# Performance work log

Hardware: AMD Instinct MI355X
Metric: run time of the kernel (lower is better)

Reference implementation:

```python
import jax, jax.numpy as jnp
import numpy as np

EPS = 1e-5  # BatchNorm eps (eval mode)
K_MAIN = 10
K_CORR = 8
LRELU = 0.2


def _knn_idx(x, k):
    # x: [B, c, n] -> [B, n, k] indices of k nearest neighbors (negative sq. distance top-k)
    inner = -2.0 * jnp.einsum('bcn,bcm->bnm', x, x)
    xx = jnp.sum(x * x, axis=1)                      # [B, n]
    pd = -xx[:, :, None] - inner - xx[:, None, :]    # [B, n, n]
    return jax.lax.top_k(pd, k)[1]


def _gather_neighbors(x, idx):
    # x: [B, c, n], idx: [B, n, k] -> [B, n, k, c]
    xt = jnp.transpose(x, (0, 2, 1))
    B = x.shape[0]
    return xt[jnp.arange(B)[:, None, None], idx]


def _graph_feature(x, k):
    # torch get_graph_feature: cat(neighbor - center, center) -> [B, 2c, n, k]
    idx = _knn_idx(x, k)
    neigh = _gather_neighbors(x, idx)                 # [B, n, k, c]
    xt = jnp.transpose(x, (0, 2, 1))                  # [B, n, c]
    center = jnp.broadcast_to(xt[:, :, None, :], neigh.shape)
    feat = jnp.concatenate([neigh - center, center], axis=-1)
    return jnp.transpose(feat, (0, 3, 1, 2))


def _branch(feat, w, g, b, m, v):
    # 1x1 Conv2d (no bias) + BatchNorm2d (eval) + LeakyReLU(0.2)
    y = jnp.einsum('oc,bcnk->bonk', w, feat)
    s = (g / jnp.sqrt(v + EPS))[None, :, None, None]
    y = (y - m[None, :, None, None]) * s + b[None, :, None, None]
    return jnp.where(y > 0, y, LRELU * y)


def _erase(x, masks, soft, w_e, b_e, g_e, be_e, m_e, v_e):
    # erase_feature: masked-softmax attention pooling + 1x1 conv_erase (conv+BN)
    soft = soft - (1.0 - masks) * 1e8
    sm = jax.nn.softmax(soft, axis=1)                 # [B, n]
    inp = x * masks[:, None, :]
    res = jnp.einsum('bcn,bn->bc', x, sm)             # [B, c]
    y = jnp.einsum('oc,bc->bo', w_e, res) + b_e
    y = (y - m_e) * (g_e / jnp.sqrt(v_e + EPS)) + be_e
    return inp + y[:, :, None]


def _corre_binar(x0_, x2, w_reduce):
    # x0_: [B, c] (detached query), x2: [B, c, n]
    B, c, n = x2.shape
    q = jnp.einsum('oc,bc->bo', w_reduce, x0_)        # conv_reduce (1x1, no bias)
    scale = 1.0 / jnp.sqrt(jnp.asarray(c, x2.dtype))
    f = jnp.einsum('bc,bcn->bn', q, x2) * scale       # [B, n]
    idx8 = _knn_idx(x2, K_CORR)                       # [B, n, 8]
    neigh = _gather_neighbors(x2, idx8)               # [B, n, 8, c]
    fk = jnp.einsum('bc,bnkc->bnk', q, neigh) * scale
    fk = f + jnp.sum(fk, axis=-1)                     # [B, n]
    index = jnp.argmax(fk, axis=1)                    # [B]
    ib = jnp.arange(B)
    masks = jnp.zeros((B, n), x2.dtype).at[ib, index].set(1.0)
    index_k = idx8[ib, index]                         # [B, 8] neighbors of argmax point
    masks = masks.at[ib[:, None], index_k].set(1.0)
    return 1.0 - masks, f


def _forward(x, w_reduce, w_erase, b_erase, g_erase, be_erase, m_erase, v_erase,
             w0, g0, b0, m0, v0, w1, g1, b1, m1, v1):
    b, t, c, n = x.shape
    B = b * t
    x1seq = jnp.concatenate([x[:, 1:], x[:, -1:]], axis=1).reshape(B, c, n)
    ones = jnp.ones((B, n), x.dtype)
    x0 = _erase(x.reshape(B, c, n), ones, ones,
                w_erase, b_erase, g_erase, be_erase, m_erase, v_erase)
    y0 = jnp.max(_branch(_graph_feature(x0, K_MAIN), w0, g0, b0, m0, v0), axis=-1)  # [B, O, n]
    x0_vec = jnp.max(y0, axis=-1)                                                    # [B, O]
    p0 = jnp.concatenate([jnp.max(y0, axis=-1), jnp.mean(y0, axis=-1)], axis=1)
    masks, soft = _corre_binar(jax.lax.stop_gradient(x0_vec), x1seq, w_reduce)
    x1e = _erase(x1seq, masks, soft,
                 w_erase, b_erase, g_erase, be_erase, m_erase, v_erase)
    y1 = jnp.max(_branch(_graph_feature(x1e, K_MAIN), w1, g1, b1, m1, v1), axis=-1)
    p1 = jnp.concatenate([jnp.max(y1, axis=-1), jnp.mean(y1, axis=-1)], axis=1)
    return p0 + p1                                                                   # [B, 2*O]


def setup_inputs() -> dict:
    key = jax.random.key(0)
    ks = jax.random.split(key, 20)
    b, t, c, n, out = 8, 12, 64, 512, 64
    sc = np.sqrt(2.0 / c).astype(np.float32)
    scb = np.sqrt(2.0 / out).astype(np.float32)
    f32 = jnp.float32
    inp = {
        'x': jax.random.normal(ks[0], (b, t, c, n), f32),
        'w_reduce': jax.random.normal(ks[1], (c, c), f32) * sc,
        'w_erase': jax.random.normal(ks[2], (c, c), f32) * sc,
        'b_erase': jax.random.normal(ks[3], (c,), f32) * 0.01,
        'g_erase': jax.random.uniform(ks[4], (c,), f32, 0.5, 1.5),
        'be_erase': jax.random.normal(ks[5], (c,), f32) * 0.1,
        'm_erase': jax.random.normal(ks[6], (c,), f32) * 0.1,
        'v_erase': jax.random.uniform(ks[7], (c,), f32, 0.5, 1.5),
        'w0': jax.random.normal(ks[8], (out, 2 * c), f32) * scb,
        'g0': jax.random.uniform(ks[9], (out,), f32, 0.5, 1.5),
        'b0': jax.random.normal(ks[10], (out,), f32) * 0.1,
        'm0': jax.random.normal(ks[11], (out,), f32) * 0.1,
        'v0': jax.random.uniform(ks[12], (out,), f32, 0.5, 1.5),
        'w1': jax.random.normal(ks[13], (out, 2 * c), f32) * scb,
        'g1': jax.random.uniform(ks[14], (out,), f32, 0.5, 1.5),
        'b1': jax.random.normal(ks[15], (out,), f32) * 0.1,
        'm1': jax.random.normal(ks[16], (out,), f32) * 0.1,
        'v1': jax.random.uniform(ks[17], (out,), f32, 0.5, 1.5),
    }
    return inp


def reference(x, w_reduce, w_erase, b_erase, g_erase, be_erase, m_erase, v_erase,
              w0, g0, b0, m0, v0, w1, g1, b1, m1, v1):
    return _forward(x, w_reduce, w_erase, b_erase, g_erase, be_erase, m_erase, v_erase,
                    w0, g0, b0, m0, v0, w1, g1, b1, m1, v1)
```

## Files before the change

kernel.cpp:

```cpp
#include <hip/hip_runtime.h>
#include <math.h>

#define EPS 1e-5f

typedef _Float16 half8 __attribute__((ext_vector_type(8)));
typedef float f32x4 __attribute__((ext_vector_type(4)));


__device__ __forceinline__ int src_row(int bq) {
    int b = bq / 12, t = bq - b * 12;
    int t2 = (t + 1 < 12) ? (t + 1) : 11;
    return b * 12 + t2;
}

__global__ __launch_bounds__(256) void prep_kernel(
    const float* __restrict__ X,
    _Float16* __restrict__ H, _Float16* __restrict__ L, float* __restrict__ xn,
    const float* __restrict__ w0, const float* __restrict__ w1,
    _Float16* __restrict__ wh0, _Float16* __restrict__ wl0,
    _Float16* __restrict__ wh1, _Float16* __restrict__ wl1,
    const float* __restrict__ w_e, const float* __restrict__ b_e,
    const float* __restrict__ g_e, const float* __restrict__ be_e,
    const float* __restrict__ m_e, const float* __restrict__ v_e,
    float* __restrict__ bias0)
{
    __shared__ float lds[64 * 65];
    __shared__ float xnp[4 * 64];
    __shared__ float part[256];
    __shared__ float res[64];
    __shared__ float sy[64];
    int raw = blockIdx.x;
    int tid = threadIdx.x;
    if (raw >= 768) {
        int bq = raw - 768;
        int c = tid >> 2, p = tid & 3;
        const float* xb = X + (size_t)bq * 32768 + c * 512 + p * 128;
        float acc = 0.f;
        for (int ii = 0; ii < 128; ii += 4) {
            float4 v = *(const float4*)(xb + ii);
            acc += v.x + v.y + v.z + v.w;
        }
        part[tid] = acc;
        __syncthreads();
        if (p == 0) res[c] = (part[tid] + part[tid+1] + part[tid+2] + part[tid+3]) * (1.f/512.f);
        __syncthreads();
        if (tid < 64) {
            float a = b_e[tid];
            for (int cc = 0; cc < 64; ++cc) a += w_e[tid*64+cc] * res[cc];
            float s = g_e[tid] / sqrtf(v_e[tid] + EPS);
            sy[tid] = (a - m_e[tid]) * s + be_e[tid];
        }
        __syncthreads();
        if (tid < 64) {
            float a = 0.f;
            for (int cc = 0; cc < 64; ++cc) a += w0[tid * 128 + 64 + cc] * sy[cc];
            bias0[bq * 64 + tid] = a;
        }
        return;
    }
    int bq = raw % 96;
    int ct = raw / 96;
    const float* Xb = X + (size_t)bq * 32768 + ct * 64;
    for (int p = 0; p < 16; ++p) {
        int t = p * 256 + tid;
        int c = t >> 6, col = t & 63;
        lds[c * 65 + col] = Xb[c * 512 + col];
    }
    __syncthreads();
    int col = tid & 63, g = tid >> 6;
    half8 hv[2], lv[2];
    float s = 0.f;
    #pragma unroll
    for (int k = 0; k < 16; ++k) {
        int c = g * 16 + k;
        float v = lds[c * 65 + col];
        _Float16 h = (_Float16)v;
        _Float16 lo = (_Float16)(v - (float)h);
        hv[k >> 3][k & 7] = h;
        lv[k >> 3][k & 7] = lo;
        s += v * v;
    }
    size_t obase = (size_t)bq * 32768 + ((size_t)(ct * 8 + 2 * g) * 64 + col) * 8;
    *(half8*)(H + obase) = hv[0];
    *(half8*)(H + obase + 512) = hv[1];
    *(half8*)(L + obase) = lv[0];
    *(half8*)(L + obase + 512) = lv[1];
    xnp[g * 64 + col] = s;
    __syncthreads();
    if (tid < 64)
        xn[bq * 512 + ct * 64 + tid] =
            xnp[tid] + xnp[64 + tid] + xnp[128 + tid] + xnp[192 + tid];
    if (raw < 2) {
        const float* W = raw ? w1 : w0;
        _Float16* WH = raw ? wh1 : wh0;
        _Float16* WL = raw ? wl1 : wl0;
        for (int t = tid; t < 8192; t += 256) {
            int o = t >> 6, c = t & 63;
            float v = (o < 64) ? W[o * 128 + c]
                               : (W[(o - 64) * 128 + 64 + c] - W[(o - 64) * 128 + c]);
            _Float16 h = (_Float16)v;
            WH[t] = h;
            WL[t] = (_Float16)(v - (float)h);
        }
    }
}

__global__ __launch_bounds__(256, 4) void knn_kernel(
    const _Float16* __restrict__ H, const _Float16* __restrict__ L,
    const float* __restrict__ xn,
    unsigned short* __restrict__ idx_out, unsigned short* __restrict__ key_out)
{
    __shared__ float4 jbuf[2048];
    __shared__ float sxn[512];
    int raw = blockIdx.x;
    int bq = raw % 96;
    int itile = raw / 96;
    int tid = threadIdx.x, w = tid >> 6, l = tid & 63;
    int lane16 = l & 15, quad = l >> 4;
    const size_t base = (size_t)bq * 32768;
    const _Float16* Hb = H + base;
    const _Float16* Lb = L + base;

    int irow = itile * 64 + w * 16 + lane16;
    size_t bo = ((size_t)(itile * 8 + quad) * 64 + (w * 16 + lane16)) * 8;
    half8 Bh0 = *(const half8*)(Hb + bo);
    half8 Bh1 = *(const half8*)(Hb + bo + 2048);
    half8 Bl0 = *(const half8*)(Lb + bo);
    half8 Bl1 = *(const half8*)(Lb + bo + 2048);

    unsigned kv[20];
    #pragma unroll
    for (int qq = 0; qq < 20; ++qq) kv[qq] = 0u;

    auto casu = [](unsigned& a, unsigned& b) {
        unsigned mn = a < b ? a : b;
        unsigned mx = a < b ? b : a;
        a = mn; b = mx;
    };

    const float* xnb = xn + bq * 512;
    float4* jbH = jbuf;
    float4* jbL = jbuf + 1024;
    {
        const float4* gh = (const float4*)(Hb);
        const float4* gl = (const float4*)(Lb);
        jbH[tid] = gh[tid]; jbH[256 + tid] = gh[256 + tid];
        jbL[tid] = gl[tid]; jbL[256 + tid] = gl[256 + tid];
        sxn[tid] = xnb[tid]; sxn[256 + tid] = xnb[256 + tid];
    }
    __syncthreads();
    for (int jt = 0; jt < 8; ++jt) {
        int cur = jt & 1;
        float4 pa0, pa1, pb0, pb1;
        if (jt < 7) {
            const float4* gh = (const float4*)(Hb + (jt + 1) * 4096);
            const float4* gl = (const float4*)(Lb + (jt + 1) * 4096);
            pa0 = gh[tid]; pa1 = gh[256 + tid];
            pb0 = gl[tid]; pb1 = gl[256 + tid];
        }
        const _Float16* jH = (const _Float16*)(jbH + cur * 512);
        const _Float16* jL = (const _Float16*)(jbL + cur * 512);
        unsigned scb = (unsigned)((7 - jt) << 4);
        unsigned d[16];
        #pragma unroll
        for (int g = 0; g < 4; ++g) {
            int u = quad * 64 + g * 16 + lane16;
            half8 Ah0 = *(const half8*)(jH + (size_t)u * 8);
            half8 Ah1 = *(const half8*)(jH + (size_t)u * 8 + 2048);
            half8 Al0 = *(const half8*)(jL + (size_t)u * 8);
            half8 Al1 = *(const half8*)(jL + (size_t)u * 8 + 2048);
            f32x4 acc = {0.f, 0.f, 0.f, 0.f};
            acc = __builtin_amdgcn_mfma_f32_16x16x32_f16(Ah0, Bh0, acc, 0, 0, 0);
            acc = __builtin_amdgcn_mfma_f32_16x16x32_f16(Ah1, Bh1, acc, 0, 0, 0);
            acc = __builtin_amdgcn_mfma_f32_16x16x32_f16(Al0, Bh0, acc, 0, 0, 0);
            acc = __builtin_amdgcn_mfma_f32_16x16x32_f16(Al1, Bh1, acc, 0, 0, 0);
            acc = __builtin_amdgcn_mfma_f32_16x16x32_f16(Ah0, Bl0, acc, 0, 0, 0);
            acc = __builtin_amdgcn_mfma_f32_16x16x32_f16(Ah1, Bl1, acc, 0, 0, 0);
            int jb = jt * 64 + g * 16 + quad * 4;
            float4 xn4 = *(const float4*)&sxn[jb];
            #pragma unroll
            for (int r = 0; r < 4; ++r) {
                float xnr = (r == 0 ? xn4.x : r == 1 ? xn4.y : r == 2 ? xn4.z : xn4.w);
                float sc = fmaf(2.f, acc[r], -xnr);
                int bi = __float_as_int(sc);
                unsigned u2 = (unsigned)(bi ^ ((bi >> 31) | 0x80000000));
                int slot = g * 4 + r;
                d[slot] = (u2 & 0xFFFFFF80u) | (scb | (unsigned)(15 - slot));
            }
        }
        #pragma unroll
        for (int p = 1; p < 16; p <<= 1) {
            #pragma unroll
            for (int k = p; k >= 1; k >>= 1) {
                #pragma unroll
                for (int j = k & (p - 1); j + k < 16; j += 2 * k) {
                    #pragma unroll
                    for (int i = 0; i < k; ++i) {
                        if ((i + j + k < 16) &&
                            ((i + j) / (2 * p) == (i + j + k) / (2 * p)))
                            casu(d[i + j], d[i + j + k]);
                    }
                }
            }
        }
        #pragma unroll
        for (int i = 0; i < 16; ++i) {
            unsigned dv = d[15 - i];
            kv[i] = kv[i] > dv ? kv[i] : dv;
        }
        casu(kv[0],kv[16]); casu(kv[1],kv[17]); casu(kv[2],kv[18]); casu(kv[3],kv[19]);
        casu(kv[0],kv[8]);  casu(kv[1],kv[9]);  casu(kv[2],kv[10]); casu(kv[3],kv[11]);
        casu(kv[4],kv[12]); casu(kv[5],kv[13]); casu(kv[6],kv[14]); casu(kv[7],kv[15]);
        casu(kv[0],kv[4]);  casu(kv[1],kv[5]);  casu(kv[2],kv[6]);  casu(kv[3],kv[7]);
        casu(kv[8],kv[12]); casu(kv[9],kv[13]); casu(kv[10],kv[14]); casu(kv[11],kv[15]);
        casu(kv[0],kv[2]);  casu(kv[1],kv[3]);  casu(kv[4],kv[6]);  casu(kv[5],kv[7]);
        casu(kv[8],kv[10]); casu(kv[9],kv[11]); casu(kv[12],kv[14]); casu(kv[13],kv[15]);
        casu(kv[16],kv[18]); casu(kv[17],kv[19]);
        casu(kv[0],kv[1]);  casu(kv[2],kv[3]);  casu(kv[4],kv[5]);  casu(kv[6],kv[7]);
        casu(kv[8],kv[9]);  casu(kv[10],kv[11]); casu(kv[12],kv[13]); casu(kv[14],kv[15]);
        casu(kv[16],kv[17]); casu(kv[18],kv[19]);

        if (jt < 7) {
            jbH[(1 - cur) * 512 + tid] = pa0; jbH[(1 - cur) * 512 + 256 + tid] = pa1;
            jbL[(1 - cur) * 512 + tid] = pb0; jbL[(1 - cur) * 512 + 256 + tid] = pb1;
        }
        __syncthreads();
    }
    unsigned* MVb = (unsigned*)jbuf;
    #pragma unroll
    for (int qq = 0; qq < 20; ++qq)
        MVb[w * 1344 + (lane16 * 4 + quad) * 21 + qq] = kv[qq];
    __syncthreads();
    if (quad == 0) {
        const unsigned* MV = (const unsigned*)jbuf + w * 1344 + lane16 * 84;
        int p0 = 19, p1 = 19, p2 = 19, p3 = 19;
        unsigned v0 = MV[19], v1 = MV[21 + 19], v2 = MV[42 + 19], v3 = MV[63 + 19];
        unsigned short* op = idx_out + ((size_t)bq * 512 + irow) * 20;
        unsigned short* kp = key_out + ((size_t)bq * 512 + irow) * 20;
        for (int t = 0; t < 20; ++t) {
            int bc = 0; unsigned bv = v0;
            if (v1 > bv) { bv = v1; bc = 1; }
            if (v2 > bv) { bv = v2; bc = 2; }
            if (v3 > bv) { bv = v3; bc = 3; }
            int bits = (int)(bv & 127u), jtv = 7 - (bits >> 4), cod = 15 - (bits & 15);
            int j = jtv * 64 + ((cod >> 2) << 4) + bc * 4 + (cod & 3);
            op[t] = (unsigned short)j;
            kp[t] = (unsigned short)(bv >> 16);
            if (bc == 0)      { --p0; v0 = MV[p0 < 0 ? 0 : p0]; }
            else if (bc == 1) { --p1; v1 = MV[21 + (p1 < 0 ? 0 : p1)]; }
            else if (bc == 2) { --p2; v2 = MV[42 + (p2 < 0 ? 0 : p2)]; }
            else              { --p3; v3 = MV[63 + (p3 < 0 ? 0 : p3)]; }
        }
    }
}

__global__ __launch_bounds__(1024) void derive_kernel(
    const float* __restrict__ x, const float* __restrict__ x0vec,
    const float* __restrict__ w_reduce,
    const unsigned short* __restrict__ idxA, const unsigned short* __restrict__ keyA,
    const float* __restrict__ xn,
    const float* __restrict__ w_e, const float* __restrict__ b_e,
    const float* __restrict__ g_e, const float* __restrict__ be_e,
    const float* __restrict__ m_e, const float* __restrict__ v_e,
    const float* __restrict__ w1,
    unsigned short* __restrict__ idxB, float* __restrict__ masks_out,
    float* __restrict__ bias1_out)
{
    __shared__ unsigned short sja[512 * 20];
    __shared__ unsigned short ska[512 * 20];
    __shared__ float ss[512];
    __shared__ float sw8[512];
    __shared__ float smask[512];
    __shared__ float xnl[512];
    __shared__ float pl[1024];
    __shared__ float sxv[64], sq[64], sres[64], syy[64];
    __shared__ float redv[8];
    __shared__ int   redi[8];
    __shared__ float redf[8];
    __shared__ float redf2[8];
    __shared__ int mlist[12];
    __shared__ int nmin[12];
    __shared__ int s_mcnt, s_need;

    int bq = blockIdx.x;
    int row = src_row(bq);
    int tid = threadIdx.x;
    int w = tid >> 6, l = tid & 63;
    const float* Xb = x + (size_t)row * 32768;

    {
        const unsigned* gja = (const unsigned*)(idxA + (size_t)row * 10240);
        const unsigned* gka = (const unsigned*)(keyA + (size_t)row * 10240);
        unsigned* dja = (unsigned*)sja;
        unsigned* dka = (unsigned*)ska;
        #pragma unroll
        for (int t = 0; t < 5; ++t) dja[t * 1024 + tid] = gja[t * 1024 + tid];
        #pragma unroll
        for (int t = 0; t < 5; ++t) dka[t * 1024 + tid] = gka[t * 1024 + tid];
    }
    if (tid < 512) { xnl[tid] = xn[row * 512 + tid]; smask[tid] = 1.0f; }
    if (tid < 64) sxv[tid] = x0vec[bq * 64 + tid];
    __syncthreads();
    {
        int o = tid >> 4, c0 = (tid & 15) * 4;
        const float* wr = w_reduce + o * 64 + c0;
        pl[tid] = wr[0]*sxv[c0] + wr[1]*sxv[c0+1] + wr[2]*sxv[c0+2] + wr[3]*sxv[c0+3];
    }
    __syncthreads();
    if (tid < 64) {
        float a = 0.f;
        #pragma unroll
        for (int s = 0; s < 16; ++s) a += pl[tid * 16 + s];
        sq[tid] = a;
    }
    __syncthreads();
    {
        int i = tid >> 1, h = tid & 1;
        float a = 0.f;
        #pragma unroll
        for (int k = 0; k < 32; ++k) {
            int c = h * 32 + k;
            a += sq[c] * Xb[c * 512 + i];
        }
        a += __shfl_xor(a, 1);
        if (h == 0) ss[i] = a * 0.125f;
    }
    __syncthreads();
    if (tid < 512) {
        float a = ss[tid];
        const unsigned short* ip = &sja[tid * 20];
        #pragma unroll
        for (int q = 0; q < 8; ++q) a += ss[ip[q]];
        sw8[tid] = a;
    }
    __syncthreads();
    {
        float bv = -3.4e38f; int bi = 0x7fffffff;
        if (tid < 512) { bv = sw8[tid]; bi = tid; }
        #pragma unroll
        for (int off = 32; off >= 1; off >>= 1) {
            float ov = __shfl_down(bv, off);
            int oi = __shfl_down(bi, off);
            if (ov > bv || (ov == bv && oi < bi)) { bv = ov; bi = oi; }
        }
        if (l == 0 && w < 8) { redv[w] = bv; redi[w] = bi; }
    }
    __syncthreads();
    if (tid == 0) {
        float Bv = redv[0]; int Bi = redi[0];
        for (int ww = 1; ww < 8; ++ww)
            if (redv[ww] > Bv || (redv[ww] == Bv && redi[ww] < Bi)) { Bv = redv[ww]; Bi = redi[ww]; }
        smask[Bi] = 0.f;
        const unsigned short* ip = &sja[Bi * 20];
        int c[9];
        c[0] = Bi;
        for (int q = 0; q < 8; ++q) { int j = ip[q]; smask[j] = 0.f; c[q + 1] = j; }
        for (int i2 = 1; i2 < 9; ++i2) {
            int v = c[i2]; int j2 = i2 - 1;
            while (j2 >= 0 && c[j2] > v) { c[j2 + 1] = c[j2]; --j2; }
            c[j2 + 1] = v;
        }
        int mc = 0, prev = -1;
        for (int i2 = 0; i2 < 9; ++i2)
            if (c[i2] != prev) { mlist[mc++] = c[i2]; prev = c[i2]; }
        s_mcnt = mc;
        s_need = 10 - mc;
    }
    __syncthreads();
    int mcreg = s_mcnt, need = s_need;
    float sval = -3.4e38f;
    if (tid < 512) {
        masks_out[bq * 512 + tid] = smask[tid];
        sval = ss[tid] - (1.f - smask[tid]) * 1e8f;
    }
    {
        float m = sval;
        #pragma unroll
        for (int off = 32; off >= 1; off >>= 1) m = fmaxf(m, __shfl_down(m, off));
        if (l == 0 && w < 8) redf[w] = m;
    }
    __syncthreads();
    float mx = fmaxf(fmaxf(fmaxf(redf[0], redf[1]), fmaxf(redf[2], redf[3])),
                     fmaxf(fmaxf(redf[4], redf[5]), fmaxf(redf[6], redf[7])));
    float ev = 0.f;
    if (tid < 512) ev = expf(sval - mx);
    {
        float s = ev;
        #pragma unroll
        for (int off = 32; off >= 1; off >>= 1) s += __shfl_down(s, off);
        if (l == 0 && w < 8) redf2[w] = s;
    }
    __syncthreads();
    {
        float sum = ((redf2[0] + redf2[1]) + (redf2[2] + redf2[3])) +
                    ((redf2[4] + redf2[5]) + (redf2[6] + redf2[7]));
        float inv = 1.f / sum;
        if (tid < 512) sw8[tid] = ev * inv;
    }
    __syncthreads();
    {
        int c = tid >> 4, sub = tid & 15;
        const float4* xr = (const float4*)(Xb + c * 512 + sub * 32);
        const float4* wr = (const float4*)(&sw8[sub * 32]);
        float a = 0.f;
        #pragma unroll
        for (int k = 0; k < 8; ++k) {
            float4 xv = xr[k], wv = wr[k];
            a += xv.x * wv.x + xv.y * wv.y + xv.z * wv.z + xv.w * wv.w;
        }
        pl[tid] = a;
    }
    __syncthreads();
    if (tid < 64) {
        float a = 0.f;
        #pragma unroll
        for (int s = 0; s < 16; ++s) a += pl[tid * 16 + s];
        sres[tid] = a;
    }
    __syncthreads();
    {
        int o = tid >> 4, c0 = (tid & 15) * 4;
        const float* wr = w_e + o * 64 + c0;
        pl[tid] = wr[0]*sres[c0] + wr[1]*sres[c0+1] + wr[2]*sres[c0+2] + wr[3]*sres[c0+3];
    }
    __syncthreads();
    if (tid < 64) {
        float a = b_e[tid];
        #pragma unroll
        for (int s = 0; s < 16; ++s) a += pl[tid * 16 + s];
        float sc2 = g_e[tid] / sqrtf(v_e[tid] + EPS);
        syy[tid] = (a - m_e[tid]) * sc2 + be_e[tid];
    }
    __syncthreads();
    {
        int o = tid >> 4, c0 = (tid & 15) * 4;
        const float* wr = w1 + o * 128 + 64 + c0;
        pl[tid] = wr[0]*syy[c0] + wr[1]*syy[c0+1] + wr[2]*syy[c0+2] + wr[3]*syy[c0+3];
    }
    __syncthreads();
    if (tid < 64) {
        float a = 0.f;
        #pragma unroll
        for (int s = 0; s < 16; ++s) a += pl[tid * 16 + s];
        bias1_out[bq * 64 + tid] = a;
    }
    for (int r = 0; r < need; ++r) {
        float bv = 3.4e38f; int bi = 0x7fffffff;
        if (tid < 512) {
            bv = (smask[tid] != 0.f) ? xnl[tid] : 3.4e38f;
            bi = tid;
        }
        #pragma unroll
        for (int off = 32; off >= 1; off >>= 1) {
            float ov = __shfl_down(bv, off);
            int oi = __shfl_down(bi, off);
            if (ov < bv || (ov == bv && oi < bi)) { bv = ov; bi = oi; }
        }
        if (l == 0 && w < 8) { redv[w] = bv; redi[w] = bi; }
        __syncthreads();
        if (tid == 0) {
            float Bv = redv[0]; int Bi = redi[0];
            for (int ww = 1; ww < 8; ++ww)
                if (redv[ww] < Bv || (redv[ww] == Bv && redi[ww] < Bi)) { Bv = redv[ww]; Bi = redi[ww]; }
            nmin[r] = Bi;
            xnl[Bi] = 3.4e38f;
        }
        __syncthreads();
    }
    if (tid < 512) {
        int i = tid;
        unsigned short tmp[10];
        if (smask[i] == 0.f) {
            int t2 = 0;
            for (int k2 = 0; k2 < mcreg; ++k2) tmp[t2++] = (unsigned short)mlist[k2];
            for (int r = 0; t2 < 10; ++r) tmp[t2++] = (unsigned short)nmin[r];
        } else {
            const unsigned short* ja = &sja[i * 20];
            const unsigned short* ka = &ska[i * 20];
            int pa = 0, pb = 0;
            for (int t2 = 0; t2 < 10; ++t2) {
                while (smask[ja[pa]] == 0.f) ++pa;
                unsigned kva = ka[pa];
                int jva = ja[pa];
                bool takeA = (pb >= mcreg) || (kva > 0x8000u) ||
                             (kva == 0x8000u && jva < mlist[pb]);
                if (takeA) { tmp[t2] = (unsigned short)jva; ++pa; }
                else       { tmp[t2] = (unsigned short)mlist[pb]; ++pb; }
            }
        }
        unsigned* op = (unsigned*)(idxB + (size_t)bq * 5120 + (size_t)i * 10);
        #pragma unroll
        for (int k2 = 0; k2 < 5; ++k2)
            op[k2] = (unsigned)tmp[2 * k2] | ((unsigned)tmp[2 * k2 + 1] << 16);
    }
}

template<int ACC>
__global__ void __attribute__((amdgpu_flat_work_group_size(256, 256), amdgpu_waves_per_eu(2, 4)))
fused_branch_kernel(
    const _Float16* __restrict__ H, const _Float16* __restrict__ L,
    const _Float16* __restrict__ WH, const _Float16* __restrict__ WL,
    const unsigned short* __restrict__ idx, int istride,
    const float* __restrict__ masks, int remap,
    const float* __restrict__ bias,
    const float* __restrict__ g, const float* __restrict__ bb,
    const float* __restrict__ mm, const float* __restrict__ vv,
    float* __restrict__ out_p, float* __restrict__ vec_out)
{
    __shared__ float ldsA[8 * 512];
    __shared__ float ldsB[8 * 512];
    __shared__ unsigned short ldsIdx[512 * 10];
    __shared__ float smask[512];
    int bq = blockIdx.x, ob = blockIdx.y * 8;
    int row = remap ? src_row(bq) : bq;
    bool use_mask = (masks != nullptr);
    int tid = threadIdx.x, w = tid >> 6, l = tid & 63;
    int lane16 = l & 15, quad = l >> 4;
    const size_t base = (size_t)row * 32768;
    unsigned idreg[10];
    if (istride == 10) {
        const unsigned* gp = (const unsigned*)idx + (size_t)bq * 2560;
        #pragma unroll
        for (int k = 0; k < 10; ++k) idreg[k] = gp[tid + k * 256];
    } else {
        const unsigned* gp = (const unsigned*)idx + (size_t)bq * 5120;
        #pragma unroll
        for (int k = 0; k < 10; ++k) {
            int d = tid + k * 256;
            int i = d / 5, r = d - i * 5;
            idreg[k] = gp[i * 10 + r];
        }
    }
    if (use_mask) {
        smask[tid] = masks[bq * 512 + tid];
        smask[tid + 256] = masks[bq * 512 + tid + 256];
        __syncthreads();
    }
    {
        int wrow = (lane16 < 8) ? (ob + lane16) : (64 + ob + (lane16 - 8));
        size_t woff = (size_t)wrow * 64 + quad * 8;
        half8 Ah0 = *(const half8*)(WH + woff);
        half8 Ah1 = *(const half8*)(WH + woff + 32);
        half8 Al0 = *(const half8*)(WL + woff);
        half8 Al1 = *(const half8*)(WL + woff + 32);
        float* dst = (quad < 2) ? (ldsA + (quad * 4) * 512) : (ldsB + ((quad - 2) * 4) * 512);
        for (int k = 0; k < 8; ++k) {
            int it = w * 8 + k;
            size_t off = base + (((size_t)(it >> 2) * 8 + quad) * 64 + (it & 3) * 16 + lane16) * 8;
            half8 Xh0 = *(const half8*)(H + off);
            half8 Xh1 = *(const half8*)(H + off + 2048);
            half8 Xl0 = *(const half8*)(L + off);
            half8 Xl1 = *(const half8*)(L + off + 2048);
            if (use_mask) {
                float m = smask[it * 16 + lane16];
                if (m == 0.f) {
                    half8 z = {};
                    Xh0 = z; Xh1 = z; Xl0 = z; Xl1 = z;
                }
            }
            f32x4 acc = {0.f, 0.f, 0.f, 0.f};
            acc = __builtin_amdgcn_mfma_f32_16x16x32_f16(Ah0, Xh0, acc, 0, 0, 0);
            acc = __builtin_amdgcn_mfma_f32_16x16x32_f16(Ah1, Xh1, acc, 0, 0, 0);
            acc = __builtin_amdgcn_mfma_f32_16x16x32_f16(Ah0, Xl0, acc, 0, 0, 0);
            acc = __builtin_amdgcn_mfma_f32_16x16x32_f16(Ah1, Xl1, acc, 0, 0, 0);
            acc = __builtin_amdgcn_mfma_f32_16x16x32_f16(Al0, Xh0, acc, 0, 0, 0);
            acc = __builtin_amdgcn_mfma_f32_16x16x32_f16(Al1, Xh1, acc, 0, 0, 0);
            #pragma unroll
            for (int r = 0; r < 4; ++r)
                dst[r * 512 + it * 16 + lane16] = acc[r];
        }
    }
    __syncthreads();
    {
        unsigned* dp = (unsigned*)ldsIdx;
        #pragma unroll
        for (int k = 0; k < 10; ++k) dp[tid + k * 256] = idreg[k];
    }
    __syncthreads();
    float ssr[2], str[2];
    #pragma unroll
    for (int oo = 0; oo < 2; ++oo) {
        int o = ob + w * 2 + oo;
        float sc = g[o] / sqrtf(vv[o] + EPS);
        ssr[oo] = sc;
        str[oo] = bb[o] - mm[o] * sc + bias[bq * 64 + o] * sc;
    }
    float omax[2], osum[2];
    #pragma unroll
    for (int oo = 0; oo < 2; ++oo) { omax[oo] = -3.4e38f; osum[oo] = 0.f; }
    const float* Aw = ldsA + (w * 2) * 512;
    const float* Bw = ldsB + (w * 2) * 512;
    for (int s = 0; s < 8; ++s) {
        int i = l + 64 * s;
        int idr[10];
        const unsigned short* ip = &ldsIdx[i * 10];
        #pragma unroll
        for (int q = 0; q < 10; ++q) idr[q] = ip[q];
        #pragma unroll
        for (int oo = 0; oo < 2; ++oo) {
            const float* Ao = Aw + oo * 512;
            float mx = Ao[idr[0]];
            #pragma unroll
            for (int q = 1; q < 10; ++q) mx = fmaxf(mx, Ao[idr[q]]);
            float val = (mx + Bw[oo * 512 + i]) * ssr[oo] + str[oo];
            float y = val > 0.f ? val : 0.2f * val;
            omax[oo] = fmaxf(omax[oo], y);
            osum[oo] += y;
        }
    }
    #pragma unroll
    for (int oo = 0; oo < 2; ++oo) {
        float M = omax[oo], S = osum[oo];
        #pragma unroll
        for (int off = 32; off >= 1; off >>= 1) {
            M = fmaxf(M, __shfl_down(M, off));
            S += __shfl_down(S, off);
        }
        if (l == 0) {
            int o = ob + w * 2 + oo;
            float* po = out_p + bq * 128;
            if (ACC) {
                po[o] += M;
                po[64 + o] += S * (1.f / 512.f);
            } else {
                po[o] = M;
                po[64 + o] = S * (1.f / 512.f);
                vec_out[bq * 64 + o] = M;
            }
        }
    }
}

extern "C" void kernel_launch(void* const* d_in, const int* in_sizes, int n_in,
                              void* d_out, int out_size, void* d_ws, size_t ws_size,
                              hipStream_t stream)
{
    const float* x        = (const float*)d_in[0];
    const float* w_reduce = (const float*)d_in[1];
    const float* w_erase  = (const float*)d_in[2];
    const float* b_erase  = (const float*)d_in[3];
    const float* g_erase  = (const float*)d_in[4];
    const float* be_erase = (const float*)d_in[5];
    const float* m_erase  = (const float*)d_in[6];
    const float* v_erase  = (const float*)d_in[7];
    const float* w0 = (const float*)d_in[8];
    const float* g0 = (const float*)d_in[9];
    const float* b0 = (const float*)d_in[10];
    const float* m0 = (const float*)d_in[11];
    const float* v0 = (const float*)d_in[12];
    const float* w1 = (const float*)d_in[13];
    const float* g1 = (const float*)d_in[14];
    const float* b1 = (const float*)d_in[15];
    const float* m1 = (const float*)d_in[16];
    const float* v1 = (const float*)d_in[17];
    float* out = (float*)d_out;
    char* ws = (char*)d_ws;

    _Float16* h0 = (_Float16*)(ws);
    _Float16* l0 = (_Float16*)(ws + 6291456);
    unsigned short* idxA = (unsigned short*)(ws + 12582912);
    unsigned short* keyA = (unsigned short*)(ws + 14548992);
    unsigned short* idxB = (unsigned short*)(ws + 16515072);
    float* xn0   = (float*)(ws + 17498112);
    float* bias0 = (float*)(ws + 17694720);
    float* bias1 = (float*)(ws + 17719296);
    float* x0vec = (float*)(ws + 17743872);
    float* masks = (float*)(ws + 17768448);
    _Float16* wh0 = (_Float16*)(ws + 17965056);
    _Float16* wl0 = (_Float16*)(ws + 17981440);
    _Float16* wh1 = (_Float16*)(ws + 17997824);
    _Float16* wl1 = (_Float16*)(ws + 18014208);

    (void)in_sizes; (void)n_in; (void)out_size; (void)ws_size;

    prep_kernel<<<864, 256, 0, stream>>>(x, h0, l0, xn0, w0, w1, wh0, wl0, wh1, wl1,
                                         w_erase, b_erase, g_erase, be_erase, m_erase, v_erase, bias0);
    knn_kernel<<<768, 256, 0, stream>>>(h0, l0, xn0, idxA, keyA);
    fused_branch_kernel<0><<<dim3(96, 8), 256, 0, stream>>>(h0, l0, wh0, wl0, idxA, 20,
                                                            nullptr, 0, bias0,
                                                            g0, b0, m0, v0, out, x0vec);
    derive_kernel<<<96, 1024, 0, stream>>>(x, x0vec, w_reduce, idxA, keyA, xn0,
                                           w_erase, b_erase, g_erase, be_erase, m_erase, v_erase,
                                           w1, idxB, masks, bias1);
    fused_branch_kernel<1><<<dim3(96, 8), 256, 0, stream>>>(h0, l0, wh1, wl1, idxB, 10,
                                                            masks, 1, bias1,
                                                            g1, b1, m1, v1, out, nullptr);
}
```

Baseline: 180.4 us.

## Interleave LDS conv outputs, single-wave min selection, and builtin min/max in sort

Replaces the block-wide iterative argmin, which used two barriers per round, with a single wavefront that keeps 8 candidates per lane and reduces with xor shuffles. Stores the MFMA outputs for output-channel pairs interleaved in LDS so the gather-max loop fetches one float2 per neighbor and reads indices as packed 32-bit words. The bitonic compare-and-swap now uses builtin elementwise min/max. One __syncthreads between the MFMA stores and the index stores is removed and the remaining barrier covers both, which relies on the two writes touching disjoint LDS.

```diff
diff --git a/kernel.cpp b/kernel.cpp
--- a/kernel.cpp
+++ b/kernel.cpp
@@ -133,8 +133,8 @@
     for (int qq = 0; qq < 20; ++qq) kv[qq] = 0u;
 
     auto casu = [](unsigned& a, unsigned& b) {
-        unsigned mn = a < b ? a : b;
-        unsigned mx = a < b ? b : a;
+        unsigned mn = __builtin_elementwise_min(a, b);
+        unsigned mx = __builtin_elementwise_max(a, b);
         a = mn; b = mx;
     };
 
@@ -204,10 +204,8 @@
             }
         }
         #pragma unroll
-        for (int i = 0; i < 16; ++i) {
-            unsigned dv = d[15 - i];
-            kv[i] = kv[i] > dv ? kv[i] : dv;
-        }
+        for (int i = 0; i < 16; ++i)
+            kv[i] = __builtin_elementwise_max(kv[i], d[15 - i]);
         casu(kv[0],kv[16]); casu(kv[1],kv[17]); casu(kv[2],kv[18]); casu(kv[3],kv[19]);
         casu(kv[0],kv[8]);  casu(kv[1],kv[9]);  casu(kv[2],kv[10]); casu(kv[3],kv[11]);
         casu(kv[4],kv[12]); casu(kv[5],kv[13]); casu(kv[6],kv[14]); casu(kv[7],kv[15]);
@@ -444,29 +442,32 @@
         for (int s = 0; s < 16; ++s) a += pl[tid * 16 + s];
         bias1_out[bq * 64 + tid] = a;
     }
-    for (int r = 0; r < need; ++r) {
-        float bv = 3.4e38f; int bi = 0x7fffffff;
-        if (tid < 512) {
-            bv = (smask[tid] != 0.f) ? xnl[tid] : 3.4e38f;
-            bi = tid;
-        }
-        #pragma unroll
-        for (int off = 32; off >= 1; off >>= 1) {
-            float ov = __shfl_down(bv, off);
-            int oi = __shfl_down(bi, off);
-            if (ov < bv || (ov == bv && oi < bi)) { bv = ov; bi = oi; }
-        }
-        if (l == 0 && w < 8) { redv[w] = bv; redi[w] = bi; }
-        __syncthreads();
-        if (tid == 0) {
-            float Bv = redv[0]; int Bi = redi[0];
-            for (int ww = 1; ww < 8; ++ww)
-                if (redv[ww] < Bv || (redv[ww] == Bv && redi[ww] < Bi)) { Bv = redv[ww]; Bi = redi[ww]; }
-            nmin[r] = Bi;
-            xnl[Bi] = 3.4e38f;
-        }
-        __syncthreads();
-    }
+    if (w == 0) {
+        float v[8]; int id[8];
+        #pragma unroll
+        for (int k = 0; k < 8; ++k) {
+            int j = l * 8 + k;
+            v[k] = (smask[j] != 0.f) ? xnl[j] : 3.4e38f;
+            id[k] = j;
+        }
+        for (int r = 0; r < need; ++r) {
+            float bv = v[0]; int bi = id[0];
+            #pragma unroll
+            for (int k = 1; k < 8; ++k)
+                if (v[k] < bv || (v[k] == bv && id[k] < bi)) { bv = v[k]; bi = id[k]; }
+            #pragma unroll
+            for (int off = 32; off >= 1; off >>= 1) {
+                float ov = __shfl_xor(bv, off);
+                int oi = __shfl_xor(bi, off);
+                if (ov < bv || (ov == bv && oi < bi)) { bv = ov; bi = oi; }
+            }
+            if (l == 0) nmin[r] = bi;
+            #pragma unroll
+            for (int k = 0; k < 8; ++k)
+                if (id[k] == bi) v[k] = 3.4e38f;
+        }
+    }
+    __syncthreads();
     if (tid < 512) {
         int i = tid;
         unsigned short tmp[10];
@@ -543,7 +544,8 @@
         half8 Ah1 = *(const half8*)(WH + woff + 32);
         half8 Al0 = *(const half8*)(WL + woff);
         half8 Al1 = *(const half8*)(WL + woff + 32);
-        float* dst = (quad < 2) ? (ldsA + (quad * 4) * 512) : (ldsB + ((quad - 2) * 4) * 512);
+        float* dst = (quad < 2) ? ldsA : ldsB;
+        int pb = (quad & 1) * 2;
         for (int k = 0; k < 8; ++k) {
             int it = w * 8 + k;
             size_t off = base + (((size_t)(it >> 2) * 8 + quad) * 64 + (it & 3) * 16 + lane16) * 8;
@@ -565,12 +567,12 @@
             acc = __builtin_amdgcn_mfma_f32_16x16x32_f16(Ah1, Xl1, acc, 0, 0, 0);
             acc = __builtin_amdgcn_mfma_f32_16x16x32_f16(Al0, Xh0, acc, 0, 0, 0);
             acc = __builtin_amdgcn_mfma_f32_16x16x32_f16(Al1, Xh1, acc, 0, 0, 0);
+            int j = it * 16 + lane16;
             #pragma unroll
             for (int r = 0; r < 4; ++r)
-                dst[r * 512 + it * 16 + lane16] = acc[r];
-        }
-    }
-    __syncthreads();
+                dst[((pb + (r >> 1)) * 512 + j) * 2 + (r & 1)] = acc[r];
+        }
+    }
     {
         unsigned* dp = (unsigned*)ldsIdx;
         #pragma unroll
@@ -588,25 +590,33 @@
     float omax[2], osum[2];
     #pragma unroll
     for (int oo = 0; oo < 2; ++oo) { omax[oo] = -3.4e38f; osum[oo] = 0.f; }
-    const float* Aw = ldsA + (w * 2) * 512;
-    const float* Bw = ldsB + (w * 2) * 512;
+    const float2* A2 = ((const float2*)ldsA) + w * 512;
+    const float2* B2 = ((const float2*)ldsB) + w * 512;
     for (int s = 0; s < 8; ++s) {
         int i = l + 64 * s;
+        const unsigned* ip32 = (const unsigned*)ldsIdx + i * 5;
+        unsigned pr0 = ip32[0], pr1 = ip32[1], pr2 = ip32[2], pr3 = ip32[3], pr4 = ip32[4];
         int idr[10];
-        const unsigned short* ip = &ldsIdx[i * 10];
-        #pragma unroll
-        for (int q = 0; q < 10; ++q) idr[q] = ip[q];
-        #pragma unroll
-        for (int oo = 0; oo < 2; ++oo) {
-            const float* Ao = Aw + oo * 512;
-            float mx = Ao[idr[0]];
-            #pragma unroll
-            for (int q = 1; q < 10; ++q) mx = fmaxf(mx, Ao[idr[q]]);
-            float val = (mx + Bw[oo * 512 + i]) * ssr[oo] + str[oo];
-            float y = val > 0.f ? val : 0.2f * val;
-            omax[oo] = fmaxf(omax[oo], y);
-            osum[oo] += y;
-        }
+        idr[0] = pr0 & 0xffff; idr[1] = pr0 >> 16;
+        idr[2] = pr1 & 0xffff; idr[3] = pr1 >> 16;
+        idr[4] = pr2 & 0xffff; idr[5] = pr2 >> 16;
+        idr[6] = pr3 & 0xffff; idr[7] = pr3 >> 16;
+        idr[8] = pr4 & 0xffff; idr[9] = pr4 >> 16;
+        float2 v0 = A2[idr[0]];
+        float mx0 = v0.x, mx1 = v0.y;
+        #pragma unroll
+        for (int q = 1; q < 10; ++q) {
+            float2 vq = A2[idr[q]];
+            mx0 = fmaxf(mx0, vq.x);
+            mx1 = fmaxf(mx1, vq.y);
+        }
+        float2 bv = B2[i];
+        float val0 = (mx0 + bv.x) * ssr[0] + str[0];
+        float val1 = (mx1 + bv.y) * ssr[1] + str[1];
+        float y0 = val0 > 0.f ? val0 : 0.2f * val0;
+        float y1 = val1 > 0.f ? val1 : 0.2f * val1;
+        omax[0] = fmaxf(omax[0], y0); osum[0] += y0;
+        omax[1] = fmaxf(omax[1], y1); osum[1] += y1;
     }
     #pragma unroll
     for (int oo = 0; oo < 2; ++oo) {
```

New measurement: 182.3 us. Within noise of the previous version (+1.1%).
